# Performance work log

Hardware: AMD Instinct MI355X
Metric: run time of the kernel (lower is better)

## Reference

```python
import jax, jax.numpy as jnp
import numpy as np
from jax import lax

B = 256; D_IN = 2048; HID = 2048; NSEG = 10; D_CTX = 1024; OUT = 100; NI = 205
KW_PCT = 0.05
K = int(round(KW_PCT * HID))  # 102 winners per sample per layer
W_DENSITY = 0.05      # weight_sparsity = 0.95
DEND_DENSITY = 0.05   # dendrite_weight_sparsity = 0.95


def setup_inputs() -> dict:
    key = jax.random.key(0)
    ks = jax.random.split(key, 16)
    def u(k, shape, bound):
        return jax.random.uniform(k, shape, minval=-bound, maxval=bound, dtype=jnp.float32)
    inp = {}
    inp["x"] = jax.random.normal(ks[0], (B, D_IN), jnp.float32)
    inp["context"] = jax.random.normal(ks[1], (B, D_CTX), jnp.float32)
    # layer 1 FF weights: modified kaiming, input density 1.0 -> bound = 1/sqrt(fan_in)
    inp["W1"] = u(ks[2], (HID, D_IN), 1.0 / np.sqrt(D_IN))
    inp["b1"] = jnp.zeros((HID,), jnp.float32)
    # dendrites: input density 1.0 (context_percent_on=1), weight density 0.05
    dend_bound = 1.0 / np.sqrt(DEND_DENSITY * D_CTX)
    inp["segW1"] = u(ks[3], (HID, NSEG, D_CTX), dend_bound)
    inp["maskW1"] = (jax.random.uniform(ks[4], (HID, D_IN)) < W_DENSITY).astype(jnp.float32)
    inp["maskS1"] = (jax.random.uniform(ks[5], (HID, NSEG, D_CTX)) < DEND_DENSITY).astype(jnp.float32)
    # layer 2 FF weights: input density = kw_percent_on (k-winners upstream)
    inp["W2"] = u(ks[6], (HID, HID), 1.0 / np.sqrt(KW_PCT * HID))
    inp["b2"] = jnp.zeros((HID,), jnp.float32)
    inp["segW2"] = u(ks[7], (HID, NSEG, D_CTX), dend_bound)
    inp["maskW2"] = (jax.random.uniform(ks[8], (HID, HID)) < W_DENSITY).astype(jnp.float32)
    inp["maskS2"] = (jax.random.uniform(ks[9], (HID, NSEG, D_CTX)) < DEND_DENSITY).astype(jnp.float32)
    # Dale (EiDense) output head: non-negative excitatory/inhibitory factors
    s = 1.0 / np.sqrt(HID)
    inp["Wex_out"] = jax.random.uniform(ks[10], (OUT, HID), dtype=jnp.float32) * s
    inp["Wix_out"] = jax.random.uniform(ks[11], (1, HID), dtype=jnp.float32) * s
    inp["Wei_out"] = jax.random.uniform(ks[12], (OUT, 1), dtype=jnp.float32)
    inp["b_out"] = jnp.zeros((OUT,), jnp.float32)
    return inp


def _kwinners(y, k):
    # keep top-k activations per row, zero the rest (boost_strength=0)
    vals, idxs = lax.top_k(y, k)  # [B, k]
    rows = jnp.arange(y.shape[0])[:, None]
    return jnp.zeros_like(y).at[rows, idxs].set(vals)


def _dendritic_layer(x, context, W, b, segW, maskW, maskS):
    # sparse-masked feedforward projection
    y = x @ (W * maskW).T + b  # [B, HID]
    # per-unit dendrite segment activations from context
    d = jnp.einsum('bc,usc->bus', context, segW * maskS)  # [B, HID, NSEG]
    # absolute-max gating: pick segment with max |activation|, gate by sigmoid
    sel = jnp.argmax(jnp.abs(d), axis=-1)  # [B, HID]
    chosen = jnp.take_along_axis(d, sel[..., None], axis=-1)[..., 0]
    y = y * jax.nn.sigmoid(chosen)
    return _kwinners(y, K)


def reference(x, context, W1, b1, segW1, maskW1, maskS1, W2, b2, segW2, maskW2, maskS2, Wex_out, Wix_out, Wei_out, b_out):
    h = _dendritic_layer(x, context, W1, b1, segW1, maskW1, maskS1)
    h = _dendritic_layer(h, context, W2, b2, segW2, maskW2, maskS2)
    # EiDense output head: W = Wex - Wei @ Wix (Dale's law), no output nonlinearity
    W_out = Wex_out - Wei_out @ Wix_out  # [OUT, HID]
    return h @ W_out.T + b_out
```

## Files before the change

kernel.cpp:

```cpp
#include <hip/hip_runtime.h>
#include <math.h>

#define B_SZ   256
#define D_IN   2048
#define HID    2048
#define NSEG   10
#define D_CTX  1024
#define OUT_N  100
#define KWIN   102
#define CAP    256

typedef float f32x4 __attribute__((ext_vector_type(4)));

__device__ __forceinline__ f32x4 ntld4(const float* p) {
  return __builtin_nontemporal_load((const f32x4*)p);
}

__device__ __forceinline__ unsigned f2key(float f) {
  unsigned b = __float_as_uint(f);
  return (b & 0x80000000u) ? ~b : (b | 0x80000000u);
}
__device__ __forceinline__ float key2f(unsigned k) {
  return (k & 0x80000000u) ? __uint_as_float(k & 0x7FFFFFFFu) : __uint_as_float(~k);
}

__global__ __launch_bounds__(256) void transpose2_k(const float* __restrict__ xsrc,
                                                    float* __restrict__ xdst,
                                                    const float* __restrict__ csrc,
                                                    float* __restrict__ cdst) {
  __shared__ float tile[32][33];
  int bid = blockIdx.x;
  const float* src; float* dst; int cols;
  const int NX = (D_IN / 32) * (B_SZ / 32);
  if (bid < NX) { src = xsrc; dst = xdst; cols = D_IN; }
  else { bid -= NX; src = csrc; dst = cdst; cols = D_CTX; }
  int nbx = cols / 32;
  int bx = bid % nbx, by = bid / nbx;
  int c0 = bx * 32, r0 = by * 32;
  int tx = threadIdx.x & 31, ty = threadIdx.x >> 5;
  for (int i = ty; i < 32; i += 8)
    tile[i][tx] = src[(r0 + i) * cols + (c0 + tx)];
  __syncthreads();
  for (int i = ty; i < 32; i += 8)
    dst[(c0 + i) * B_SZ + (r0 + tx)] = tile[tx][i];
}

__device__ __forceinline__ int compact_wave(const float* __restrict__ wrow,
                                            const float* __restrict__ mrow,
                                            int len4, float2* pairs, int* scnt) {
  const int t = threadIdx.x & 63;
  if (t == 0) *scnt = 0;
  __builtin_amdgcn_wave_barrier();
  for (int e = t; e < len4; e += 64) {
    f32x4 w = ntld4(wrow + 4 * e);
    f32x4 m = ntld4(mrow + 4 * e);
    bool n0 = (m.x != 0.f), n1 = (m.y != 0.f), n2 = (m.z != 0.f), n3 = (m.w != 0.f);
    int nz = (int)n0 + (int)n1 + (int)n2 + (int)n3;
    if (nz) {
      int pos = atomicAdd(scnt, nz);
      int c = e << 2;
      if (n0) { if (pos < CAP) pairs[pos] = make_float2(w.x, __int_as_float(c));     pos++; }
      if (n1) { if (pos < CAP) pairs[pos] = make_float2(w.y, __int_as_float(c + 1)); pos++; }
      if (n2) { if (pos < CAP) pairs[pos] = make_float2(w.z, __int_as_float(c + 2)); pos++; }
      if (n3) { if (pos < CAP) pairs[pos] = make_float2(w.w, __int_as_float(c + 3)); pos++; }
    }
  }
  __builtin_amdgcn_wave_barrier();
  int c = *scnt;
  return c > CAP ? CAP : c;
}

__device__ __forceinline__ int store_seg(const f32x4 w[4], const f32x4 m[4],
                                         float2* pairs, int* scnt) {
  const int t = threadIdx.x & 63;
  if (t == 0) *scnt = 0;
  __builtin_amdgcn_wave_barrier();
#pragma unroll
  for (int i = 0; i < 4; ++i) {
    int e = t + 64 * i;
    f32x4 ww = w[i], mm = m[i];
    bool n0 = (mm.x != 0.f), n1 = (mm.y != 0.f), n2 = (mm.z != 0.f), n3 = (mm.w != 0.f);
    int nz = (int)n0 + (int)n1 + (int)n2 + (int)n3;
    if (nz) {
      int pos = atomicAdd(scnt, nz);
      int c = e << 2;
      if (n0) { if (pos < CAP) pairs[pos] = make_float2(ww.x, __int_as_float(c));     pos++; }
      if (n1) { if (pos < CAP) pairs[pos] = make_float2(ww.y, __int_as_float(c + 1)); pos++; }
      if (n2) { if (pos < CAP) pairs[pos] = make_float2(ww.z, __int_as_float(c + 2)); pos++; }
      if (n3) { if (pos < CAP) pairs[pos] = make_float2(ww.w, __int_as_float(c + 3)); pos++; }
    }
  }
  __builtin_amdgcn_wave_barrier();
  int c = *scnt;
  return c > CAP ? CAP : c;
}

__device__ __forceinline__ void load_seg(const float* __restrict__ wrow,
                                         const float* __restrict__ mrow,
                                         f32x4 w[4], f32x4 m[4]) {
  const int t = threadIdx.x & 63;
#pragma unroll
  for (int i = 0; i < 4; ++i) {
    w[i] = ntld4(wrow + 4 * (t + 64 * i));
    m[i] = ntld4(mrow + 4 * (t + 64 * i));
  }
}

__device__ __forceinline__ void gather_dot(const float* __restrict__ src,
                                           const float2* pairs, int cnt,
                                           int t4, float out4[4]) {
  float acc[4][4];
#pragma unroll
  for (int s = 0; s < 4; ++s)
#pragma unroll
    for (int i = 0; i < 4; ++i) acc[s][i] = 0.f;
  int j = 0;
  for (; j + 8 <= cnt; j += 8) {
#pragma unroll
    for (int s = 0; s < 8; ++s) {
      float2 p = pairs[j + s];
      const f32x4 cv = *(const f32x4*)(src + (__float_as_int(p.y) << 8) + t4);
      acc[s & 3][0] += cv.x * p.x; acc[s & 3][1] += cv.y * p.x;
      acc[s & 3][2] += cv.z * p.x; acc[s & 3][3] += cv.w * p.x;
    }
  }
  for (; j < cnt; ++j) {
    float2 p = pairs[j];
    const f32x4 cv = *(const f32x4*)(src + (__float_as_int(p.y) << 8) + t4);
    acc[0][0] += cv.x * p.x; acc[0][1] += cv.y * p.x;
    acc[0][2] += cv.z * p.x; acc[0][3] += cv.w * p.x;
  }
#pragma unroll
  for (int i = 0; i < 4; ++i)
    out4[i] = (acc[0][i] + acc[1][i]) + (acc[2][i] + acc[3][i]);
}

__global__ __launch_bounds__(256, 3) void dend_kernel(
    const float* __restrict__ W1, const float* __restrict__ maskW1, const float* __restrict__ b1,
    const float* __restrict__ segW1, const float* __restrict__ maskS1,
    const float* __restrict__ segW2, const float* __restrict__ maskS2,
    const float* __restrict__ xT, const float* __restrict__ ctxT,
    float* __restrict__ y1T, float* __restrict__ gate2T) {
  __shared__ float2 pairs_s[4][CAP];
  __shared__ int scnt_s[4];
  const int wave = threadIdx.x >> 6;
  const int t = threadIdx.x & 63, t4 = t * 4;
  float2* pairs = pairs_s[wave];
  int* scnt = &scnt_s[wave];
  const int row = blockIdx.x * 4 + wave;

  const bool isL1 = (row < HID);
  const int u = isL1 ? row : (row - HID);
  const float* segW = (isL1 ? segW1 : segW2) + (size_t)u * NSEG * D_CTX;
  const float* maskS = (isL1 ? maskS1 : maskS2) + (size_t)u * NSEG * D_CTX;

  float bestA[4] = {-1.f, -1.f, -1.f, -1.f};
  float chosen[4] = {0.f, 0.f, 0.f, 0.f};
  float ff[4] = {0.f, 0.f, 0.f, 0.f};

  f32x4 w[4], m[4];
  if (isL1) {
    int cnt = compact_wave(W1 + (size_t)u * D_IN, maskW1 + (size_t)u * D_IN,
                           D_IN / 4, pairs, scnt);
    load_seg(segW, maskS, w, m);
    gather_dot(xT, pairs, cnt, t4, ff);
  } else {
    load_seg(segW, maskS, w, m);
  }

  for (int s = 0; s < NSEG; ++s) {
    int cnt = store_seg(w, m, pairs, scnt);
    if (s + 1 < NSEG)
      load_seg(segW + (s + 1) * D_CTX, maskS + (s + 1) * D_CTX, w, m);
    float d[4];
    gather_dot(ctxT, pairs, cnt, t4, d);
#pragma unroll
    for (int i = 0; i < 4; ++i) {
      float a = fabsf(d[i]);
      if (a > bestA[i]) { bestA[i] = a; chosen[i] = d[i]; }
    }
  }

  if (isL1) {
    float bb = b1[u];
    float4 o;
    o.x = (ff[0] + bb) / (1.f + expf(-chosen[0]));
    o.y = (ff[1] + bb) / (1.f + expf(-chosen[1]));
    o.z = (ff[2] + bb) / (1.f + expf(-chosen[2]));
    o.w = (ff[3] + bb) / (1.f + expf(-chosen[3]));
    *(float4*)(y1T + (size_t)u * B_SZ + t4) = o;
  } else {
    float4 g;
    g.x = 1.f / (1.f + expf(-chosen[0]));
    g.y = 1.f / (1.f + expf(-chosen[1]));
    g.z = 1.f / (1.f + expf(-chosen[2]));
    g.w = 1.f / (1.f + expf(-chosen[3]));
    *(float4*)(gate2T + (size_t)u * B_SZ + t4) = g;
  }
}

__global__ __launch_bounds__(256, 4) void ff2_kernel(
    const float* __restrict__ W2, const float* __restrict__ maskW2, const float* __restrict__ b2,
    const float* __restrict__ h1T, const float* __restrict__ gate2T, float* __restrict__ y2T) {
  __shared__ float2 pairs_s[4][CAP];
  __shared__ int scnt_s[4];
  const int wave = threadIdx.x >> 6;
  const int t = threadIdx.x & 63, t4 = t * 4;
  const int u = blockIdx.x * 4 + wave;
  int cnt = compact_wave(W2 + (size_t)u * HID, maskW2 + (size_t)u * HID,
                         HID / 4, pairs_s[wave], &scnt_s[wave]);
  float acc[4];
  gather_dot(h1T, pairs_s[wave], cnt, t4, acc);
  float bb = b2[u];
  float4 g = *(const float4*)(gate2T + (size_t)u * B_SZ + t4);
  float4 o;
  o.x = (acc[0] + bb) * g.x; o.y = (acc[1] + bb) * g.y;
  o.z = (acc[2] + bb) * g.z; o.w = (acc[3] + bb) * g.w;
  *(float4*)(y2T + (size_t)u * B_SZ + t4) = o;
}

__global__ __launch_bounds__(256) void topk_kernel(const float* __restrict__ yT,
                                                   float* __restrict__ dst, int mode) {
  const int b = blockIdx.x, t = threadIdx.x;
  __shared__ int hist[256];
  __shared__ int sfx[256];
  __shared__ unsigned sPref;
  __shared__ int sRem;
  unsigned myk[8];
#pragma unroll
  for (int i = 0; i < 8; ++i)
    myk[i] = f2key(yT[(size_t)(t * 8 + i) * B_SZ + b]);
  unsigned pref = 0;
  int rem = KWIN;
  for (int shift = 24; shift >= 0; shift -= 8) {
    hist[t] = 0;
    __syncthreads();
    unsigned hiMask = (shift == 24) ? 0u : (0xFFFFFFFFu << (shift + 8));
#pragma unroll
    for (int i = 0; i < 8; ++i) {
      unsigned k = myk[i];
      if ((k & hiMask) == pref) atomicAdd(&hist[(k >> shift) & 255], 1);
    }
    __syncthreads();
    sfx[t] = hist[t];
    __syncthreads();
    for (int off = 1; off < 256; off <<= 1) {
      int add = (t + off < 256) ? sfx[t + off] : 0;
      __syncthreads();
      sfx[t] += add;
      __syncthreads();
    }
    int s_incl = sfx[t];
    int s_excl = (t == 255) ? 0 : sfx[t + 1];
    if (s_incl >= rem && s_excl < rem) {
      sPref = pref | (((unsigned)t) << shift);
      sRem = rem - s_excl;
    }
    __syncthreads();
    pref = sPref;
    rem = sRem;
    __syncthreads();
  }
  int eq = 0;
#pragma unroll
  for (int i = 0; i < 8; ++i) eq += (myk[i] == pref) ? 1 : 0;
  sfx[t] = eq;
  __syncthreads();
  for (int off = 1; off < 256; off <<= 1) {
    int add = (t >= off) ? sfx[t - off] : 0;
    __syncthreads();
    sfx[t] += add;
    __syncthreads();
  }
  int excl = sfx[t] - eq;
  int taken = 0;
#pragma unroll
  for (int i = 0; i < 8; ++i) {
    unsigned k = myk[i];
    bool keep;
    if (k > pref) keep = true;
    else if (k == pref) { keep = (excl + taken) < rem; taken++; }
    else keep = false;
    float f = keep ? key2f(k) : 0.f;
    int uu = t * 8 + i;
    if (mode == 0) dst[(size_t)uu * B_SZ + b] = f;
    else dst[(size_t)b * HID + uu] = f;
  }
}

__global__ __launch_bounds__(256) void out_kernel(
    const float* __restrict__ h2, const float* __restrict__ Wex, const float* __restrict__ Wix,
    const float* __restrict__ Wei, const float* __restrict__ bo, float* __restrict__ out) {
  const int b = blockIdx.x, t = threadIdx.x;
  __shared__ float hrow[HID];
  __shared__ float red[256];
  float part = 0.f;
#pragma unroll
  for (int i = 0; i < 8; ++i) {
    int u = t + 256 * i;
    float v = h2[(size_t)b * HID + u];
    hrow[u] = v;
    part += v * Wix[u];
  }
  red[t] = part;
  __syncthreads();
  for (int off = 128; off > 0; off >>= 1) {
    if (t < off) red[t] += red[t + off];
    __syncthreads();
  }
  float S = red[0];
  const int w = t >> 6, l = t & 63;
  for (int o = w; o < OUT_N; o += 4) {
    float acc = 0.f;
    const float* wr = Wex + (size_t)o * HID;
#pragma unroll
    for (int q = 0; q < HID / 64; ++q) acc += hrow[l + 64 * q] * wr[l + 64 * q];
    for (int off = 32; off > 0; off >>= 1) acc += __shfl_down(acc, off, 64);
    if (l == 0) out[(size_t)b * OUT_N + o] = acc - Wei[o] * S + bo[o];
  }
}

extern "C" void kernel_launch(void* const* d_in, const int* in_sizes, int n_in,
                              void* d_out, int out_size, void* d_ws, size_t ws_size,
                              hipStream_t stream) {
  const float* x      = (const float*)d_in[0];
  const float* ctx    = (const float*)d_in[1];
  const float* W1     = (const float*)d_in[2];
  const float* b1     = (const float*)d_in[3];
  const float* segW1  = (const float*)d_in[4];
  const float* maskW1 = (const float*)d_in[5];
  const float* maskS1 = (const float*)d_in[6];
  const float* W2     = (const float*)d_in[7];
  const float* b2     = (const float*)d_in[8];
  const float* segW2  = (const float*)d_in[9];
  const float* maskW2 = (const float*)d_in[10];
  const float* maskS2 = (const float*)d_in[11];
  const float* Wex    = (const float*)d_in[12];
  const float* Wix    = (const float*)d_in[13];
  const float* Wei    = (const float*)d_in[14];
  const float* bo     = (const float*)d_in[15];
  float* out = (float*)d_out;
  float* ws = (float*)d_ws;

  float* xT     = ws;
  float* ctxT   = ws + 524288;
  float* y1T    = ws + 786432;
  float* gate2T = ws + 1310720;
  float* y2T    = ws + 1835008;
  float* h2     = ws + 2359296;

  transpose2_k<<<768, 256, 0, stream>>>(x, xT, ctx, ctxT);
  dend_kernel<<<2 * HID / 4, 256, 0, stream>>>(W1, maskW1, b1, segW1, maskS1, segW2, maskS2,
                                               xT, ctxT, y1T, gate2T);
  topk_kernel<<<B_SZ, 256, 0, stream>>>(y1T, y1T, 0);
  ff2_kernel<<<HID / 4, 256, 0, stream>>>(W2, maskW2, b2, y1T, gate2T, y2T);
  topk_kernel<<<B_SZ, 256, 0, stream>>>(y2T, h2, 1);
  out_kernel<<<B_SZ, 256, 0, stream>>>(h2, Wex, Wix, Wei, bo, out);
}
```

Baseline: 496.0 us.

## Split sparse compaction into separate kernels and compute dendrite gates from LDS-tiled context

Replaces the fused dendrite kernel with separate passes. One pass compacts masked segment weights and one compacts masked FF weights into global (value, index) lists. A new dendgate kernel stages a 16-column context tile in LDS and computes segment dot products from shared memory instead of gathering from global ctxT. A generic ffgate kernel then applies the FF gather and gate for both layers. This is meant to raise parallelism and data reuse for the dendrite stage, at the cost of extra launches and global round-trips for the compacted lists. It also adds lower per-row capacity caps (96 and 160 entries), which risk truncating rows with more nonzeros than expected.

```diff
diff --git a/kernel.cpp b/kernel.cpp
--- a/kernel.cpp
+++ b/kernel.cpp
@@ -8,7 +8,9 @@
 #define D_CTX  1024
 #define OUT_N  100
 #define KWIN   102
-#define CAP    256
+#define CAPS   96
+#define CAPF   160
+#define NCT    16
 
 typedef float f32x4 __attribute__((ext_vector_type(4)));
 
@@ -45,70 +47,144 @@
     dst[(c0 + i) * B_SZ + (r0 + tx)] = tile[tx][i];
 }
 
-__device__ __forceinline__ int compact_wave(const float* __restrict__ wrow,
-                                            const float* __restrict__ mrow,
-                                            int len4, float2* pairs, int* scnt) {
+template<int PER, int CAP>
+__device__ __forceinline__ void compact_row(const float* __restrict__ w,
+                                            const float* __restrict__ mk,
+                                            float2* __restrict__ outP,
+                                            int* __restrict__ outC,
+                                            float2* buf, int* scnt) {
   const int t = threadIdx.x & 63;
+  f32x4 wv[PER], mv[PER];
+#pragma unroll
+  for (int i = 0; i < PER; ++i) {
+    wv[i] = ntld4(w + 4 * (t + 64 * i));
+    mv[i] = ntld4(mk + 4 * (t + 64 * i));
+  }
   if (t == 0) *scnt = 0;
   __builtin_amdgcn_wave_barrier();
-  for (int e = t; e < len4; e += 64) {
-    f32x4 w = ntld4(wrow + 4 * e);
-    f32x4 m = ntld4(mrow + 4 * e);
-    bool n0 = (m.x != 0.f), n1 = (m.y != 0.f), n2 = (m.z != 0.f), n3 = (m.w != 0.f);
-    int nz = (int)n0 + (int)n1 + (int)n2 + (int)n3;
-    if (nz) {
-      int pos = atomicAdd(scnt, nz);
-      int c = e << 2;
-      if (n0) { if (pos < CAP) pairs[pos] = make_float2(w.x, __int_as_float(c));     pos++; }
-      if (n1) { if (pos < CAP) pairs[pos] = make_float2(w.y, __int_as_float(c + 1)); pos++; }
-      if (n2) { if (pos < CAP) pairs[pos] = make_float2(w.z, __int_as_float(c + 2)); pos++; }
-      if (n3) { if (pos < CAP) pairs[pos] = make_float2(w.w, __int_as_float(c + 3)); pos++; }
-    }
-  }
-  __builtin_amdgcn_wave_barrier();
-  int c = *scnt;
-  return c > CAP ? CAP : c;
-}
-
-__device__ __forceinline__ int store_seg(const f32x4 w[4], const f32x4 m[4],
-                                         float2* pairs, int* scnt) {
-  const int t = threadIdx.x & 63;
-  if (t == 0) *scnt = 0;
-  __builtin_amdgcn_wave_barrier();
-#pragma unroll
-  for (int i = 0; i < 4; ++i) {
+#pragma unroll
+  for (int i = 0; i < PER; ++i) {
     int e = t + 64 * i;
-    f32x4 ww = w[i], mm = m[i];
+    f32x4 ww = wv[i], mm = mv[i];
     bool n0 = (mm.x != 0.f), n1 = (mm.y != 0.f), n2 = (mm.z != 0.f), n3 = (mm.w != 0.f);
     int nz = (int)n0 + (int)n1 + (int)n2 + (int)n3;
     if (nz) {
       int pos = atomicAdd(scnt, nz);
       int c = e << 2;
-      if (n0) { if (pos < CAP) pairs[pos] = make_float2(ww.x, __int_as_float(c));     pos++; }
-      if (n1) { if (pos < CAP) pairs[pos] = make_float2(ww.y, __int_as_float(c + 1)); pos++; }
-      if (n2) { if (pos < CAP) pairs[pos] = make_float2(ww.z, __int_as_float(c + 2)); pos++; }
-      if (n3) { if (pos < CAP) pairs[pos] = make_float2(ww.w, __int_as_float(c + 3)); pos++; }
+      if (n0) { if (pos < CAP) buf[pos] = make_float2(ww.x, __int_as_float(c));     pos++; }
+      if (n1) { if (pos < CAP) buf[pos] = make_float2(ww.y, __int_as_float(c + 1)); pos++; }
+      if (n2) { if (pos < CAP) buf[pos] = make_float2(ww.z, __int_as_float(c + 2)); pos++; }
+      if (n3) { if (pos < CAP) buf[pos] = make_float2(ww.w, __int_as_float(c + 3)); pos++; }
     }
   }
   __builtin_amdgcn_wave_barrier();
   int c = *scnt;
-  return c > CAP ? CAP : c;
-}
-
-__device__ __forceinline__ void load_seg(const float* __restrict__ wrow,
-                                         const float* __restrict__ mrow,
-                                         f32x4 w[4], f32x4 m[4]) {
-  const int t = threadIdx.x & 63;
-#pragma unroll
-  for (int i = 0; i < 4; ++i) {
-    w[i] = ntld4(wrow + 4 * (t + 64 * i));
-    m[i] = ntld4(mrow + 4 * (t + 64 * i));
-  }
-}
-
-__device__ __forceinline__ void gather_dot(const float* __restrict__ src,
-                                           const float2* pairs, int cnt,
-                                           int t4, float out4[4]) {
+  if (c > CAP) c = CAP;
+  for (int i = t; i < c; i += 64) outP[i] = buf[i];
+  if (t == 0) *outC = c;
+}
+
+__global__ __launch_bounds__(256, 4) void compact_ff_k(
+    const float* __restrict__ W1, const float* __restrict__ mW1,
+    const float* __restrict__ W2, const float* __restrict__ mW2,
+    float2* __restrict__ ff1P, int* __restrict__ ff1C,
+    float2* __restrict__ ff2P, int* __restrict__ ff2C) {
+  __shared__ float2 buf_s[4][CAPF];
+  __shared__ int cnt_s[4];
+  int wave = threadIdx.x >> 6;
+  int rid = blockIdx.x * 4 + wave;
+  if (rid < HID)
+    compact_row<8, CAPF>(W1 + (size_t)rid * D_IN, mW1 + (size_t)rid * D_IN,
+                         ff1P + (size_t)rid * CAPF, ff1C + rid, buf_s[wave], &cnt_s[wave]);
+  else {
+    int u = rid - HID;
+    compact_row<8, CAPF>(W2 + (size_t)u * HID, mW2 + (size_t)u * HID,
+                         ff2P + (size_t)u * CAPF, ff2C + u, buf_s[wave], &cnt_s[wave]);
+  }
+}
+
+__global__ __launch_bounds__(256, 4) void compact_seg_k(
+    const float* __restrict__ segW1, const float* __restrict__ mS1,
+    const float* __restrict__ segW2, const float* __restrict__ mS2,
+    float2* __restrict__ segP, int* __restrict__ segC) {
+  __shared__ float2 buf_s[4][CAPS];
+  __shared__ int cnt_s[4];
+  int wave = threadIdx.x >> 6;
+  int rid = blockIdx.x * 4 + wave;
+  const float *w, *mk;
+  if (rid < HID * NSEG) {
+    w = segW1 + (size_t)rid * D_CTX;  mk = mS1 + (size_t)rid * D_CTX;
+  } else {
+    int loc = rid - HID * NSEG;
+    w = segW2 + (size_t)loc * D_CTX;  mk = mS2 + (size_t)loc * D_CTX;
+  }
+  compact_row<4, CAPS>(w, mk, segP + (size_t)rid * CAPS, segC + rid,
+                       buf_s[wave], &cnt_s[wave]);
+}
+
+__global__ __launch_bounds__(256) void dendgate_k(
+    const float2* __restrict__ segP, const int* __restrict__ segC,
+    const float* __restrict__ ctxT, float* __restrict__ gateT) {
+  __shared__ float ctx_lds[D_CTX * NCT];
+  const int tile = blockIdx.x & 15;
+  const int chunk = blockIdx.x >> 4;
+  const int b0 = tile * NCT;
+  {
+    int tt = threadIdx.x;
+    int cq = (tt & 3) * 4;
+    for (int r = tt >> 2; r < D_CTX; r += 64) {
+      f32x4 v = *(const f32x4*)(ctxT + (size_t)r * B_SZ + b0 + cq);
+      *(f32x4*)(&ctx_lds[r * NCT + cq]) = v;
+    }
+  }
+  __syncthreads();
+  const int wave = threadIdx.x >> 6;
+  const int l = threadIdx.x & 63;
+  const int c = l & 15, g = l >> 4;
+  for (int k = 0; k < 32; ++k) {
+    int rowid = chunk * 128 + wave * 32 + k;
+    const float2* __restrict__ prow = segP + (size_t)rowid * NSEG * CAPS;
+    const int* __restrict__ crow = segC + rowid * NSEG;
+    int cnts[NSEG];
+#pragma unroll
+    for (int s = 0; s < NSEG; ++s) cnts[s] = crow[s];
+    float bestA = -1.f, chosen = 0.f;
+#pragma unroll 1
+    for (int s = 0; s < NSEG; ++s) {
+      const float2* __restrict__ pr = prow + s * CAPS;
+      int cnt = cnts[s];
+      float d0 = 0.f, d1 = 0.f, d2 = 0.f, d3 = 0.f;
+      int j = g;
+      for (; j + 12 < cnt; j += 16) {
+        float2 pa = pr[j], pb = pr[j + 4], pc = pr[j + 8], pd = pr[j + 12];
+        d0 += ctx_lds[__float_as_int(pa.y) * NCT + c] * pa.x;
+        d1 += ctx_lds[__float_as_int(pb.y) * NCT + c] * pb.x;
+        d2 += ctx_lds[__float_as_int(pc.y) * NCT + c] * pc.x;
+        d3 += ctx_lds[__float_as_int(pd.y) * NCT + c] * pd.x;
+      }
+      for (; j < cnt; j += 4) {
+        float2 p = pr[j];
+        d0 += ctx_lds[__float_as_int(p.y) * NCT + c] * p.x;
+      }
+      float d = (d0 + d1) + (d2 + d3);
+      d += __shfl_xor(d, 16, 64);
+      d += __shfl_xor(d, 32, 64);
+      float a = fabsf(d);
+      if (a > bestA) { bestA = a; chosen = d; }
+    }
+    float gate = 1.f / (1.f + expf(-chosen));
+    if (l < NCT) gateT[(size_t)rowid * B_SZ + b0 + c] = gate;
+  }
+}
+
+__global__ __launch_bounds__(256, 4) void ffgate_k(
+    const float2* __restrict__ P, const int* __restrict__ C,
+    const float* __restrict__ srcT, const float* __restrict__ gate,
+    const float* __restrict__ bias, float* __restrict__ yT) {
+  int wave = threadIdx.x >> 6, t = threadIdx.x & 63, t4 = t * 4;
+  int u = blockIdx.x * 4 + wave;
+  const float2* __restrict__ pr = P + (size_t)u * CAPF;
+  int cnt = C[u];
   float acc[4][4];
 #pragma unroll
   for (int s = 0; s < 4; ++s)
@@ -118,105 +194,26 @@
   for (; j + 8 <= cnt; j += 8) {
 #pragma unroll
     for (int s = 0; s < 8; ++s) {
-      float2 p = pairs[j + s];
-      const f32x4 cv = *(const f32x4*)(src + (__float_as_int(p.y) << 8) + t4);
+      float2 p = pr[j + s];
+      const f32x4 cv = *(const f32x4*)(srcT + ((size_t)__float_as_int(p.y) << 8) + t4);
       acc[s & 3][0] += cv.x * p.x; acc[s & 3][1] += cv.y * p.x;
       acc[s & 3][2] += cv.z * p.x; acc[s & 3][3] += cv.w * p.x;
     }
   }
   for (; j < cnt; ++j) {
-    float2 p = pairs[j];
-    const f32x4 cv = *(const f32x4*)(src + (__float_as_int(p.y) << 8) + t4);
+    float2 p = pr[j];
+    const f32x4 cv = *(const f32x4*)(srcT + ((size_t)__float_as_int(p.y) << 8) + t4);
     acc[0][0] += cv.x * p.x; acc[0][1] += cv.y * p.x;
     acc[0][2] += cv.z * p.x; acc[0][3] += cv.w * p.x;
   }
-#pragma unroll
-  for (int i = 0; i < 4; ++i)
-    out4[i] = (acc[0][i] + acc[1][i]) + (acc[2][i] + acc[3][i]);
-}
-
-__global__ __launch_bounds__(256, 3) void dend_kernel(
-    const float* __restrict__ W1, const float* __restrict__ maskW1, const float* __restrict__ b1,
-    const float* __restrict__ segW1, const float* __restrict__ maskS1,
-    const float* __restrict__ segW2, const float* __restrict__ maskS2,
-    const float* __restrict__ xT, const float* __restrict__ ctxT,
-    float* __restrict__ y1T, float* __restrict__ gate2T) {
-  __shared__ float2 pairs_s[4][CAP];
-  __shared__ int scnt_s[4];
-  const int wave = threadIdx.x >> 6;
-  const int t = threadIdx.x & 63, t4 = t * 4;
-  float2* pairs = pairs_s[wave];
-  int* scnt = &scnt_s[wave];
-  const int row = blockIdx.x * 4 + wave;
-
-  const bool isL1 = (row < HID);
-  const int u = isL1 ? row : (row - HID);
-  const float* segW = (isL1 ? segW1 : segW2) + (size_t)u * NSEG * D_CTX;
-  const float* maskS = (isL1 ? maskS1 : maskS2) + (size_t)u * NSEG * D_CTX;
-
-  float bestA[4] = {-1.f, -1.f, -1.f, -1.f};
-  float chosen[4] = {0.f, 0.f, 0.f, 0.f};
-  float ff[4] = {0.f, 0.f, 0.f, 0.f};
-
-  f32x4 w[4], m[4];
-  if (isL1) {
-    int cnt = compact_wave(W1 + (size_t)u * D_IN, maskW1 + (size_t)u * D_IN,
-                           D_IN / 4, pairs, scnt);
-    load_seg(segW, maskS, w, m);
-    gather_dot(xT, pairs, cnt, t4, ff);
-  } else {
-    load_seg(segW, maskS, w, m);
-  }
-
-  for (int s = 0; s < NSEG; ++s) {
-    int cnt = store_seg(w, m, pairs, scnt);
-    if (s + 1 < NSEG)
-      load_seg(segW + (s + 1) * D_CTX, maskS + (s + 1) * D_CTX, w, m);
-    float d[4];
-    gather_dot(ctxT, pairs, cnt, t4, d);
-#pragma unroll
-    for (int i = 0; i < 4; ++i) {
-      float a = fabsf(d[i]);
-      if (a > bestA[i]) { bestA[i] = a; chosen[i] = d[i]; }
-    }
-  }
-
-  if (isL1) {
-    float bb = b1[u];
-    float4 o;
-    o.x = (ff[0] + bb) / (1.f + expf(-chosen[0]));
-    o.y = (ff[1] + bb) / (1.f + expf(-chosen[1]));
-    o.z = (ff[2] + bb) / (1.f + expf(-chosen[2]));
-    o.w = (ff[3] + bb) / (1.f + expf(-chosen[3]));
-    *(float4*)(y1T + (size_t)u * B_SZ + t4) = o;
-  } else {
-    float4 g;
-    g.x = 1.f / (1.f + expf(-chosen[0]));
-    g.y = 1.f / (1.f + expf(-chosen[1]));
-    g.z = 1.f / (1.f + expf(-chosen[2]));
-    g.w = 1.f / (1.f + expf(-chosen[3]));
-    *(float4*)(gate2T + (size_t)u * B_SZ + t4) = g;
-  }
-}
-
-__global__ __launch_bounds__(256, 4) void ff2_kernel(
-    const float* __restrict__ W2, const float* __restrict__ maskW2, const float* __restrict__ b2,
-    const float* __restrict__ h1T, const float* __restrict__ gate2T, float* __restrict__ y2T) {
-  __shared__ float2 pairs_s[4][CAP];
-  __shared__ int scnt_s[4];
-  const int wave = threadIdx.x >> 6;
-  const int t = threadIdx.x & 63, t4 = t * 4;
-  const int u = blockIdx.x * 4 + wave;
-  int cnt = compact_wave(W2 + (size_t)u * HID, maskW2 + (size_t)u * HID,
-                         HID / 4, pairs_s[wave], &scnt_s[wave]);
-  float acc[4];
-  gather_dot(h1T, pairs_s[wave], cnt, t4, acc);
-  float bb = b2[u];
-  float4 g = *(const float4*)(gate2T + (size_t)u * B_SZ + t4);
+  float bb = bias[u];
+  float4 g4 = *(const float4*)(gate + (size_t)u * B_SZ + t4);
   float4 o;
-  o.x = (acc[0] + bb) * g.x; o.y = (acc[1] + bb) * g.y;
-  o.z = (acc[2] + bb) * g.z; o.w = (acc[3] + bb) * g.w;
-  *(float4*)(y2T + (size_t)u * B_SZ + t4) = o;
+  o.x = ((acc[0][0] + acc[1][0]) + (acc[2][0] + acc[3][0]) + bb) * g4.x;
+  o.y = ((acc[0][1] + acc[1][1]) + (acc[2][1] + acc[3][1]) + bb) * g4.y;
+  o.z = ((acc[0][2] + acc[1][2]) + (acc[2][2] + acc[3][2]) + bb) * g4.z;
+  o.w = ((acc[0][3] + acc[1][3]) + (acc[2][3] + acc[3][3]) + bb) * g4.w;
+  *(float4*)(yT + (size_t)u * B_SZ + t4) = o;
 }
 
 __global__ __launch_bounds__(256) void topk_kernel(const float* __restrict__ yT,
@@ -342,18 +339,28 @@
   float* out = (float*)d_out;
   float* ws = (float*)d_ws;
 
-  float* xT     = ws;
-  float* ctxT   = ws + 524288;
-  float* y1T    = ws + 786432;
-  float* gate2T = ws + 1310720;
-  float* y2T    = ws + 1835008;
-  float* h2     = ws + 2359296;
+  float*  xT    = ws;
+  float*  ctxT  = ws + 524288;
+  float*  y1T   = ws + 786432;
+  float*  y2T   = ws + 1310720;
+  float*  h2    = ws + 1835008;
+  float*  gateT = ws + 2359296;
+  float2* segP  = (float2*)(ws + 3407872);
+  float2* ff1P  = (float2*)(ws + 11272192);
+  float2* ff2P  = (float2*)(ws + 11927552);
+  int*    segC  = (int*)(ws + 12582912);
+  int*    ff1C  = (int*)(ws + 12623872);
+  int*    ff2C  = (int*)(ws + 12625920);
 
   transpose2_k<<<768, 256, 0, stream>>>(x, xT, ctx, ctxT);
-  dend_kernel<<<2 * HID / 4, 256, 0, stream>>>(W1, maskW1, b1, segW1, maskS1, segW2, maskS2,
-                                               xT, ctxT, y1T, gate2T);
+  compact_seg_k<<<2 * HID * NSEG / 4, 256, 0, stream>>>(segW1, maskS1, segW2, maskS2,
+                                                        segP, segC);
+  dendgate_k<<<512, 256, 0, stream>>>(segP, segC, ctxT, gateT);
+  compact_ff_k<<<2 * HID / 4, 256, 0, stream>>>(W1, maskW1, W2, maskW2,
+                                                ff1P, ff1C, ff2P, ff2C);
+  ffgate_k<<<HID / 4, 256, 0, stream>>>(ff1P, ff1C, xT, gateT, b1, y1T);
   topk_kernel<<<B_SZ, 256, 0, stream>>>(y1T, y1T, 0);
-  ff2_kernel<<<HID / 4, 256, 0, stream>>>(W2, maskW2, b2, y1T, gate2T, y2T);
+  ffgate_k<<<HID / 4, 256, 0, stream>>>(ff2P, ff2C, y1T, gateT + (size_t)HID * B_SZ, b2, y2T);
   topk_kernel<<<B_SZ, 256, 0, stream>>>(y2T, h2, 1);
   out_kernel<<<B_SZ, 256, 0, stream>>>(h2, Wex, Wix, Wei, bo, out);
 }
```

After: 997.2 us. 101% more time.
